# Kernel optimization log

Hardware: AMD Instinct MI355X
Metric: run time of the kernel (lower is better)

## Reference

```python
import jax, jax.numpy as jnp
import numpy as np

B = 8192
I_SIZE = 1024
H_SIZE = 1024
C2 = 2.7183  # module's hard-coded e approximation

def setup_inputs() -> dict:
    key = jax.random.key(0)
    k0, k1, k2, k3, k4 = jax.random.split(key, 5)
    input_tensor = jax.random.uniform(k0, (B, I_SIZE + 1), dtype=jnp.float32)  # last col = dt >= 0
    h_cur = jax.random.normal(k1, (B, H_SIZE), dtype=jnp.float32)
    c_cur = jax.random.normal(k2, (B, H_SIZE), dtype=jnp.float32)
    W_layers = jax.random.normal(k3, (4 * H_SIZE, I_SIZE + H_SIZE), dtype=jnp.float32) * 0.02
    b_layers = jnp.zeros((4 * H_SIZE,), dtype=jnp.float32)
    W_desc = jax.random.normal(k4, (H_SIZE, H_SIZE), dtype=jnp.float32) * 0.02
    b_desc = jnp.zeros((H_SIZE,), dtype=jnp.float32)
    return {"input_tensor": input_tensor, "h_cur": h_cur, "c_cur": c_cur,
            "W_layers": W_layers, "b_layers": b_layers,
            "W_desc": W_desc, "b_desc": b_desc}

def reference(input_tensor, h_cur, c_cur, W_layers, b_layers, W_desc, b_desc):
    x = input_tensor[:, :-1]          # [B, I]
    dt = input_tensor[:, -1:]         # [B, 1]
    # map_elapse_time: T = 1/log(t + e), broadcast over h_size (matmul with ones == broadcast)
    T = 1.0 / jnp.log(dt + C2)        # [B, 1]
    C_ST = jnp.tanh(h_cur @ W_desc.T + b_desc)          # [B, H]
    h_adj = h_cur - C_ST + T * C_ST                     # decayed short-term memory
    combined = jnp.concatenate([x, h_adj], axis=1)      # [B, I+H]
    gates = combined @ W_layers.T + b_layers            # [B, 4H]
    cc_i, cc_f, cc_o, cc_g = jnp.split(gates, 4, axis=1)
    i = jax.nn.sigmoid(cc_i)
    f = jax.nn.sigmoid(cc_f)
    o = jax.nn.sigmoid(cc_o)
    g = jnp.tanh(cc_g)
    c_next = f * c_cur + i * g
    h_next = o * jnp.tanh(c_next)
    return (h_next, c_next)
```

## Files before the change

### kernel.cpp

```cpp
#include <hip/hip_runtime.h>
#include <hip/hip_bf16.h>
#include <math.h>

typedef __bf16 bf16x8 __attribute__((ext_vector_type(8)));
typedef float  f32x4  __attribute__((ext_vector_type(4)));

#define B_ROWS 8192
#define HSZ    1024

#define GLOAD16(gsrc, ldst)                                                          \
  __builtin_amdgcn_global_load_lds((const __attribute__((address_space(1))) void*)(gsrc), \
                                   (__attribute__((address_space(3))) void*)(ldst),  \
                                   16, 0, 0)

__device__ inline unsigned short f2bf(float f) {
  union { float f; unsigned u; } x; x.f = f;
  unsigned r = x.u + 0x7fffu + ((x.u >> 16) & 1u);
  return (unsigned short)(r >> 16);
}

__device__ inline void store4bf(unsigned short* p, float4 v) {
  ushort4 u;
  u.x = f2bf(v.x); u.y = f2bf(v.y); u.z = f2bf(v.z); u.w = f2bf(v.w);
  *(ushort4*)p = u;
}

__device__ inline float sigm(float x) { return 1.0f / (1.0f + __expf(-x)); }

__global__ void k_convert(const float* __restrict__ inp,
                          const float* __restrict__ h,
                          const float* __restrict__ Wl,
                          const float* __restrict__ Wd,
                          unsigned short* __restrict__ comb,
                          unsigned short* __restrict__ Wlb,
                          unsigned short* __restrict__ hb,
                          unsigned short* __restrict__ Wdb,
                          float* __restrict__ Tm1) {
  const long stride = (long)gridDim.x * blockDim.x;
  const long tid0 = (long)blockIdx.x * blockDim.x + threadIdx.x;

  for (long i = tid0; i < (long)B_ROWS * HSZ / 4; i += stride) {
    float4 v = ((const float4*)h)[i];
    store4bf(hb + i * 4, v);
  }
  for (long i = tid0; i < (long)B_ROWS * HSZ / 4; i += stride) {
    long e = i * 4; long b = e >> 10; long c = e & 1023;
    float4 v = *(const float4*)(inp + b * 1025 + c);
    store4bf(comb + b * 2048 + c, v);
  }
  for (long i = tid0; i < 4096L * 2048 / 4; i += stride) {
    float4 v = ((const float4*)Wl)[i];
    store4bf(Wlb + i * 4, v);
  }
  for (long i = tid0; i < 1024L * 1024 / 4; i += stride) {
    float4 v = ((const float4*)Wd)[i];
    store4bf(Wdb + i * 4, v);
  }
  for (long i = tid0; i < B_ROWS; i += stride) {
    float dt = inp[i * 1025 + 1024];
    Tm1[i] = 1.0f / logf(dt + 2.7183f) - 1.0f;
  }
}

__global__ void k_gemm1(const unsigned short* __restrict__ A,
                        const unsigned short* __restrict__ Bm,
                        const float* __restrict__ h,
                        const float* __restrict__ bd,
                        const float* __restrict__ Tm1,
                        unsigned short* __restrict__ comb) {
  const int K = 1024;
  __shared__ __align__(16) unsigned short As[128 * 32];
  __shared__ __align__(16) unsigned short Bs[128 * 32];
  const int tid = threadIdx.x;
  const int lane = tid & 63;
  const int wave = tid >> 6;
  const int wr = wave >> 1, wc = wave & 1;
  const int bRow = blockIdx.x;
  const int bCol = blockIdx.y;

  const int sRow = tid >> 2;
  const int sK = (tid & 3) * 8;
  const unsigned short* aSrc0 = A + (long)(bRow * 128 + sRow) * K + sK;
  const unsigned short* aSrc1 = A + (long)(bRow * 128 + 64 + sRow) * K + sK;
  const unsigned short* bSrc0 = Bm + (long)(bCol * 128 + sRow) * K + sK;
  const unsigned short* bSrc1 = Bm + (long)(bCol * 128 + 64 + sRow) * K + sK;
  unsigned short* aDst0 = As + tid * 8;
  unsigned short* aDst1 = As + 2048 + tid * 8;
  unsigned short* bDst0 = Bs + tid * 8;
  unsigned short* bDst1 = Bs + 2048 + tid * 8;

  f32x4 acc[4][4] = {};
  const int fr = lane & 15, fk = (lane >> 4) * 8;

  for (int k0 = 0; k0 < K; k0 += 32) {
    GLOAD16(aSrc0 + k0, aDst0);
    GLOAD16(aSrc1 + k0, aDst1);
    GLOAD16(bSrc0 + k0, bDst0);
    GLOAD16(bSrc1 + k0, bDst1);
    __syncthreads();
    bf16x8 a[4], b[4];
#pragma unroll
    for (int m = 0; m < 4; m++) a[m] = *(const bf16x8*)(As + (wr * 64 + m * 16 + fr) * 32 + fk);
#pragma unroll
    for (int n = 0; n < 4; n++) b[n] = *(const bf16x8*)(Bs + (wc * 64 + n * 16 + fr) * 32 + fk);
#pragma unroll
    for (int m = 0; m < 4; m++)
#pragma unroll
      for (int n = 0; n < 4; n++)
        acc[m][n] = __builtin_amdgcn_mfma_f32_16x16x32_bf16(a[m], b[n], acc[m][n], 0, 0, 0);
    __syncthreads();
  }

  const int cr = (lane >> 4) * 4;
  const int cc = lane & 15;
#pragma unroll
  for (int m = 0; m < 4; m++)
#pragma unroll
    for (int n = 0; n < 4; n++) {
      const int col = bCol * 128 + wc * 64 + n * 16 + cc;
#pragma unroll
      for (int r = 0; r < 4; r++) {
        const int row = bRow * 128 + wr * 64 + m * 16 + cr + r;
        float v = acc[m][n][r] + bd[col];
        float cst = tanhf(v);
        float hadj = h[(long)row * HSZ + col] + Tm1[row] * cst;
        comb[(long)row * 2048 + 1024 + col] = f2bf(hadj);
      }
    }
}

#define NT2 64
__global__ __launch_bounds__(512, 2)
void k_gemm2_fr(const unsigned short* __restrict__ A,
                const unsigned short* __restrict__ Bm,
                const float* __restrict__ bl,
                const float* __restrict__ c_cur,
                float* __restrict__ out) {
  __shared__ __align__(16) unsigned short lds[4][16384];

  const int tid = threadIdx.x;
  const int lane = tid & 63;
  const int wid = tid >> 6;
  const int wr = wid >> 2;
  const int wc = wid & 3;

  const int bid = blockIdx.x;
  const int xcd = bid & 7;
  const int ii = bid >> 3;
  const int sweep = ii >> 5;
  const int pos = ii & 31;
  const int bRow = xcd * 4 + sweep * 2 + (pos & 1);
  const int bCol = pos >> 1;

  const int sr = tid >> 2;
  const int swsel = (sr >> 1) & 3;
  const int gk = ((tid & 3) ^ swsel) << 3;
  const unsigned short* aBase = A + (long)(bRow * 256 + sr) * 2048 + gk;
  const int rl0 = sr, rl1 = 128 + sr;
  const int grow0 = ((rl0 >> 4) & 3) * 1024 + bCol * 64 + (rl0 >> 6) * 16 + (rl0 & 15);
  const int grow1 = ((rl1 >> 4) & 3) * 1024 + bCol * 64 + (rl1 >> 6) * 16 + (rl1 & 15);
  const unsigned short* bBase0 = Bm + (long)grow0 * 2048 + gk;
  const unsigned short* bBase1 = Bm + (long)grow1 * 2048 + gk;

#define STAGE_A2(slot, tt) { unsigned short* d_ = &lds[slot][0] + tid * 8;        \
    GLOAD16(aBase + (long)(tt) * 32, d_);                                          \
    GLOAD16(aBase + 128L * 2048 + (long)(tt) * 32, d_ + 512 * 8); }
#define STAGE_B2(slot, tt) { unsigned short* d_ = &lds[slot][8192] + tid * 8;     \
    GLOAD16(bBase0 + (long)(tt) * 32, d_);                                         \
    GLOAD16(bBase1 + (long)(tt) * 32, d_ + 512 * 8); }

  const int fr = lane & 15, q = lane >> 4;
  int offA[8], offB[4];
#pragma unroll
  for (int m = 0; m < 8; m++) {
    const int row = wr * 128 + m * 16 + fr;
    offA[m] = row * 32 + ((q ^ ((row >> 1) & 3)) << 3);
  }
#pragma unroll
  for (int n = 0; n < 4; n++) {
    const int row = wc * 64 + n * 16 + fr;
    offB[n] = 8192 + row * 32 + ((q ^ ((row >> 1) & 3)) << 3);
  }

  f32x4 acc[8][4] = {};

  STAGE_A2(0, 0); STAGE_B2(0, 0);
  STAGE_A2(1, 1); STAGE_B2(1, 1);
  STAGE_A2(2, 2); STAGE_B2(2, 2);

#define BODY(t, SLOT, VM, DOSTAGE)                                                   \
  {                                                                                  \
    asm volatile("s_waitcnt vmcnt(" #VM ")" ::: "memory");                           \
    __builtin_amdgcn_s_barrier();                                                    \
    if (DOSTAGE) { STAGE_A2(((t) + 3) & 3, (t) + 3); STAGE_B2(((t) + 3) & 3, (t) + 3); } \
    const unsigned short* buf = &lds[SLOT][0];                                       \
    bf16x8 aF[8], bF[4];                                                             \
    _Pragma("unroll")                                                                \
    for (int n = 0; n < 4; n++) bF[n] = *(const bf16x8*)(buf + offB[n]);             \
    _Pragma("unroll")                                                                \
    for (int m = 0; m < 8; m++) aF[m] = *(const bf16x8*)(buf + offA[m]);             \
    __builtin_amdgcn_s_setprio(1);                                                   \
    _Pragma("unroll")                                                                \
    for (int m = 0; m < 8; m++)                                                      \
      _Pragma("unroll")                                                              \
      for (int n = 0; n < 4; n++)                                                    \
        acc[m][n] = __builtin_amdgcn_mfma_f32_16x16x32_bf16(aF[m], bF[n], acc[m][n], 0, 0, 0); \
    __builtin_amdgcn_s_setprio(0);                                                   \
  }

  for (int t = 0; t < 60; t += 4) {
    BODY(t,     0, 8, true);
    BODY(t + 1, 1, 8, true);
    BODY(t + 2, 2, 8, true);
    BODY(t + 3, 3, 8, true);
  }
  BODY(60, 0, 8, true);
  BODY(61, 1, 8, false);
  BODY(62, 2, 4, false);
  BODY(63, 3, 0, false);
#undef BODY

  const int cr = (lane >> 4) * 4;
  const int cc = lane & 15;
  const int j = bCol * 64 + wc * 16 + cc;
#pragma unroll
  for (int m = 0; m < 8; m++) {
#pragma unroll
    for (int r = 0; r < 4; r++) {
      const int row = bRow * 256 + wr * 128 + m * 16 + cr + r;
      float iv = sigm(acc[m][0][r] + bl[j]);
      float fv = sigm(acc[m][1][r] + bl[1024 + j]);
      float ov = sigm(acc[m][2][r] + bl[2048 + j]);
      float gv = tanhf(acc[m][3][r] + bl[3072 + j]);
      float cn = fv * c_cur[(long)row * HSZ + j] + iv * gv;
      float hn = ov * tanhf(cn);
      out[(long)row * HSZ + j] = hn;
      out[(long)B_ROWS * HSZ + (long)row * HSZ + j] = cn;
    }
  }
}

extern "C" void kernel_launch(void* const* d_in, const int* in_sizes, int n_in,
                              void* d_out, int out_size, void* d_ws, size_t ws_size,
                              hipStream_t stream) {
  const float* inp = (const float*)d_in[0];
  const float* h   = (const float*)d_in[1];
  const float* c   = (const float*)d_in[2];
  const float* Wl  = (const float*)d_in[3];
  const float* bl  = (const float*)d_in[4];
  const float* Wd  = (const float*)d_in[5];
  const float* bd  = (const float*)d_in[6];

  char* ws = (char*)d_ws;
  unsigned short* comb = (unsigned short*)(ws);
  unsigned short* Wlb  = (unsigned short*)(ws + 33554432);
  unsigned short* hb   = (unsigned short*)(ws + 50331648);
  unsigned short* Wdb  = (unsigned short*)(ws + 67108864);
  float*          Tm1  = (float*)(ws + 69206016);
  float*          out  = (float*)d_out;

  hipLaunchKernelGGL(k_convert, dim3(2048), dim3(256), 0, stream,
                     inp, h, Wl, Wd, comb, Wlb, hb, Wdb, Tm1);
  hipLaunchKernelGGL(k_gemm1, dim3(64, 8), dim3(256), 0, stream,
                     hb, Wdb, h, bd, Tm1, comb);
  hipLaunchKernelGGL(k_gemm2_fr, dim3(512), dim3(512), 0, stream,
                     comb, Wlb, bl, c, out);
}
```

Before: 226.2 us.

## Switch gates GEMM to 32x32x16 MFMA with 4x2 wave layout, widen convert loads

Rewrites the main gates GEMM to use 32x32x16 bf16 MFMA instead of 16x16x32, rearranging the waves as 4 rows by 2 columns, each computing 64 rows by 32 columns for every one of the four gates. B-tile staging and the LDS fragment offsets are remapped so each gate's 64 columns sit contiguously. The epilogue is adapted to the 32x32 accumulator layout and hoists the bias loads. The convert kernel also handles 8 elements per thread iteration instead of 4. Larger MFMA tiles need fewer LDS fragment reads per FLOP, at the cost of a new fragment mapping that could hit bank conflicts or be wrong.

```diff
diff --git a/kernel.cpp b/kernel.cpp
--- a/kernel.cpp
+++ b/kernel.cpp
@@ -4,6 +4,7 @@
 
 typedef __bf16 bf16x8 __attribute__((ext_vector_type(8)));
 typedef float  f32x4  __attribute__((ext_vector_type(4)));
+typedef float  f32x16 __attribute__((ext_vector_type(16)));
 
 #define B_ROWS 8192
 #define HSZ    1024
@@ -17,12 +18,6 @@
   union { float f; unsigned u; } x; x.f = f;
   unsigned r = x.u + 0x7fffu + ((x.u >> 16) & 1u);
   return (unsigned short)(r >> 16);
-}
-
-__device__ inline void store4bf(unsigned short* p, float4 v) {
-  ushort4 u;
-  u.x = f2bf(v.x); u.y = f2bf(v.y); u.z = f2bf(v.z); u.w = f2bf(v.w);
-  *(ushort4*)p = u;
 }
 
 __device__ inline float sigm(float x) { return 1.0f / (1.0f + __expf(-x)); }
@@ -39,27 +34,34 @@
   const long stride = (long)gridDim.x * blockDim.x;
   const long tid0 = (long)blockIdx.x * blockDim.x + threadIdx.x;
 
-  for (long i = tid0; i < (long)B_ROWS * HSZ / 4; i += stride) {
-    float4 v = ((const float4*)h)[i];
-    store4bf(hb + i * 4, v);
-  }
-  for (long i = tid0; i < (long)B_ROWS * HSZ / 4; i += stride) {
-    long e = i * 4; long b = e >> 10; long c = e & 1023;
-    float4 v = *(const float4*)(inp + b * 1025 + c);
-    store4bf(comb + b * 2048 + c, v);
-  }
-  for (long i = tid0; i < 4096L * 2048 / 4; i += stride) {
-    float4 v = ((const float4*)Wl)[i];
-    store4bf(Wlb + i * 4, v);
-  }
-  for (long i = tid0; i < 1024L * 1024 / 4; i += stride) {
-    float4 v = ((const float4*)Wd)[i];
-    store4bf(Wdb + i * 4, v);
+#define CNV8(dst, s0, s1) { ushort4 u0, u1;                                   \
+    u0.x = f2bf(s0.x); u0.y = f2bf(s0.y); u0.z = f2bf(s0.z); u0.w = f2bf(s0.w); \
+    u1.x = f2bf(s1.x); u1.y = f2bf(s1.y); u1.z = f2bf(s1.z); u1.w = f2bf(s1.w); \
+    *(ushort4*)(dst) = u0; *(ushort4*)((dst) + 4) = u1; }
+
+  for (long i = tid0; i < (long)B_ROWS * HSZ / 8; i += stride) {
+    float4 v0 = ((const float4*)h)[i * 2], v1 = ((const float4*)h)[i * 2 + 1];
+    CNV8(hb + i * 8, v0, v1);
+  }
+  for (long i = tid0; i < (long)B_ROWS * HSZ / 8; i += stride) {
+    long e = i * 8; long b = e >> 10; long c = e & 1023;
+    const float* s = inp + b * 1025 + c;
+    float4 v0 = *(const float4*)s, v1 = *(const float4*)(s + 4);
+    CNV8(comb + b * 2048 + c, v0, v1);
+  }
+  for (long i = tid0; i < 4096L * 2048 / 8; i += stride) {
+    float4 v0 = ((const float4*)Wl)[i * 2], v1 = ((const float4*)Wl)[i * 2 + 1];
+    CNV8(Wlb + i * 8, v0, v1);
+  }
+  for (long i = tid0; i < 1024L * 1024 / 8; i += stride) {
+    float4 v0 = ((const float4*)Wd)[i * 2], v1 = ((const float4*)Wd)[i * 2 + 1];
+    CNV8(Wdb + i * 8, v0, v1);
   }
   for (long i = tid0; i < B_ROWS; i += stride) {
     float dt = inp[i * 1025 + 1024];
     Tm1[i] = 1.0f / logf(dt + 2.7183f) - 1.0f;
   }
+#undef CNV8
 }
 
 __global__ void k_gemm1(const unsigned short* __restrict__ A,
@@ -131,7 +133,7 @@
 
 #define NT2 64
 __global__ __launch_bounds__(512, 2)
-void k_gemm2_fr(const unsigned short* __restrict__ A,
+void k_gemm2_32(const unsigned short* __restrict__ A,
                 const unsigned short* __restrict__ Bm,
                 const float* __restrict__ bl,
                 const float* __restrict__ c_cur,
@@ -141,8 +143,8 @@
   const int tid = threadIdx.x;
   const int lane = tid & 63;
   const int wid = tid >> 6;
-  const int wr = wid >> 2;
-  const int wc = wid & 3;
+  const int wr = wid >> 1;
+  const int wc = wid & 1;
 
   const int bid = blockIdx.x;
   const int xcd = bid & 7;
@@ -156,33 +158,35 @@
   const int swsel = (sr >> 1) & 3;
   const int gk = ((tid & 3) ^ swsel) << 3;
   const unsigned short* aBase = A + (long)(bRow * 256 + sr) * 2048 + gk;
-  const int rl0 = sr, rl1 = 128 + sr;
-  const int grow0 = ((rl0 >> 4) & 3) * 1024 + bCol * 64 + (rl0 >> 6) * 16 + (rl0 & 15);
-  const int grow1 = ((rl1 >> 4) & 3) * 1024 + bCol * 64 + (rl1 >> 6) * 16 + (rl1 & 15);
+  const int grow0 = (sr >> 6) * 1024 + bCol * 64 + (sr & 63);
+  const int grow1 = (2 + (sr >> 6)) * 1024 + bCol * 64 + (sr & 63);
   const unsigned short* bBase0 = Bm + (long)grow0 * 2048 + gk;
   const unsigned short* bBase1 = Bm + (long)grow1 * 2048 + gk;
 
 #define STAGE_A2(slot, tt) { unsigned short* d_ = &lds[slot][0] + tid * 8;        \
     GLOAD16(aBase + (long)(tt) * 32, d_);                                          \
-    GLOAD16(aBase + 128L * 2048 + (long)(tt) * 32, d_ + 512 * 8); }
+    GLOAD16(aBase + 128L * 2048 + (long)(tt) * 32, d_ + 4096); }
 #define STAGE_B2(slot, tt) { unsigned short* d_ = &lds[slot][8192] + tid * 8;     \
     GLOAD16(bBase0 + (long)(tt) * 32, d_);                                         \
-    GLOAD16(bBase1 + (long)(tt) * 32, d_ + 512 * 8); }
-
-  const int fr = lane & 15, q = lane >> 4;
-  int offA[8], offB[4];
-#pragma unroll
-  for (int m = 0; m < 8; m++) {
-    const int row = wr * 128 + m * 16 + fr;
-    offA[m] = row * 32 + ((q ^ ((row >> 1) & 3)) << 3);
-  }
-#pragma unroll
-  for (int n = 0; n < 4; n++) {
-    const int row = wc * 64 + n * 16 + fr;
-    offB[n] = 8192 + row * 32 + ((q ^ ((row >> 1) & 3)) << 3);
-  }
-
-  f32x4 acc[8][4] = {};
+    GLOAD16(bBase1 + (long)(tt) * 32, d_ + 4096); }
+
+  int offA[2][2], offB[4][2];
+#pragma unroll
+  for (int mt = 0; mt < 2; mt++)
+#pragma unroll
+    for (int ks = 0; ks < 2; ks++) {
+      const int row = wr * 64 + mt * 32 + (lane & 31);
+      offA[mt][ks] = row * 32 + (((2 * ks + (lane >> 5)) ^ ((row >> 1) & 3)) << 3);
+    }
+#pragma unroll
+  for (int g = 0; g < 4; g++)
+#pragma unroll
+    for (int ks = 0; ks < 2; ks++) {
+      const int rl = g * 64 + wc * 32 + (lane & 31);
+      offB[g][ks] = 8192 + rl * 32 + (((2 * ks + (lane >> 5)) ^ ((rl >> 1) & 3)) << 3);
+    }
+
+  f32x16 acc[2][4] = {};
 
   STAGE_A2(0, 0); STAGE_B2(0, 0);
   STAGE_A2(1, 1); STAGE_B2(1, 1);
@@ -194,17 +198,25 @@
     __builtin_amdgcn_s_barrier();                                                    \
     if (DOSTAGE) { STAGE_A2(((t) + 3) & 3, (t) + 3); STAGE_B2(((t) + 3) & 3, (t) + 3); } \
     const unsigned short* buf = &lds[SLOT][0];                                       \
-    bf16x8 aF[8], bF[4];                                                             \
+    bf16x8 aF[2][2], bF[4][2];                                                       \
     _Pragma("unroll")                                                                \
-    for (int n = 0; n < 4; n++) bF[n] = *(const bf16x8*)(buf + offB[n]);             \
+    for (int g = 0; g < 4; g++) {                                                    \
+      bF[g][0] = *(const bf16x8*)(buf + offB[g][0]);                                 \
+      bF[g][1] = *(const bf16x8*)(buf + offB[g][1]);                                 \
+    }                                                                                \
     _Pragma("unroll")                                                                \
-    for (int m = 0; m < 8; m++) aF[m] = *(const bf16x8*)(buf + offA[m]);             \
+    for (int mt = 0; mt < 2; mt++) {                                                 \
+      aF[mt][0] = *(const bf16x8*)(buf + offA[mt][0]);                               \
+      aF[mt][1] = *(const bf16x8*)(buf + offA[mt][1]);                               \
+    }                                                                                \
     __builtin_amdgcn_s_setprio(1);                                                   \
     _Pragma("unroll")                                                                \
-    for (int m = 0; m < 8; m++)                                                      \
+    for (int mt = 0; mt < 2; mt++)                                                   \
       _Pragma("unroll")                                                              \
-      for (int n = 0; n < 4; n++)                                                    \
-        acc[m][n] = __builtin_amdgcn_mfma_f32_16x16x32_bf16(aF[m], bF[n], acc[m][n], 0, 0, 0); \
+      for (int g = 0; g < 4; g++) {                                                  \
+        acc[mt][g] = __builtin_amdgcn_mfma_f32_32x32x16_bf16(aF[mt][0], bF[g][0], acc[mt][g], 0, 0, 0); \
+        acc[mt][g] = __builtin_amdgcn_mfma_f32_32x32x16_bf16(aF[mt][1], bF[g][1], acc[mt][g], 0, 0, 0); \
+      }                                                                              \
     __builtin_amdgcn_s_setprio(0);                                                   \
   }
 
@@ -220,18 +232,18 @@
   BODY(63, 3, 0, false);
 #undef BODY
 
-  const int cr = (lane >> 4) * 4;
-  const int cc = lane & 15;
-  const int j = bCol * 64 + wc * 16 + cc;
-#pragma unroll
-  for (int m = 0; m < 8; m++) {
-#pragma unroll
-    for (int r = 0; r < 4; r++) {
-      const int row = bRow * 256 + wr * 128 + m * 16 + cr + r;
-      float iv = sigm(acc[m][0][r] + bl[j]);
-      float fv = sigm(acc[m][1][r] + bl[1024 + j]);
-      float ov = sigm(acc[m][2][r] + bl[2048 + j]);
-      float gv = tanhf(acc[m][3][r] + bl[3072 + j]);
+  const int j = bCol * 64 + wc * 32 + (lane & 31);
+  const int rb = (lane >> 5) * 4;
+  const float bl0 = bl[j], bl1 = bl[1024 + j], bl2 = bl[2048 + j], bl3 = bl[3072 + j];
+#pragma unroll
+  for (int mt = 0; mt < 2; mt++) {
+#pragma unroll
+    for (int r = 0; r < 16; r++) {
+      const int row = bRow * 256 + wr * 64 + mt * 32 + (r & 3) + 8 * (r >> 2) + rb;
+      float iv = sigm(acc[mt][0][r] + bl0);
+      float fv = sigm(acc[mt][1][r] + bl1);
+      float ov = sigm(acc[mt][2][r] + bl2);
+      float gv = tanhf(acc[mt][3][r] + bl3);
       float cn = fv * c_cur[(long)row * HSZ + j] + iv * gv;
       float hn = ov * tanhf(cn);
       out[(long)row * HSZ + j] = hn;
@@ -263,6 +275,6 @@
                      inp, h, Wl, Wd, comb, Wlb, hb, Wdb, Tm1);
   hipLaunchKernelGGL(k_gemm1, dim3(64, 8), dim3(256), 0, stream,
                      hb, Wdb, h, bd, Tm1, comb);
-  hipLaunchKernelGGL(k_gemm2_fr, dim3(512), dim3(512), 0, stream,
+  hipLaunchKernelGGL(k_gemm2_32, dim3(512), dim3(512), 0, stream,
                      comb, Wlb, bl, c, out);
 }
```

Result: slower. 247.4 us (+9.4%).

## Switch gemm2 to paired-stage pipeline with fewer barriers; widen convert loops

Applied to the files above, without the earlier changes.

The main GEMM moves from a 4-slot ring with prefetch depth 3 and one barrier per K-step to a scheme that processes two K-steps per barrier. It prefetches two stages ahead into the other half of the LDS buffers and drains vmcnt to zero at each pair boundary. The conversion kernel now handles 8 floats per thread iteration instead of 4. The aim is to halve barrier count and cut loop overhead, at the cost of a shallower prefetch and full memory drains that may expose load latency.

```diff
diff --git a/kernel.cpp b/kernel.cpp
--- a/kernel.cpp
+++ b/kernel.cpp
@@ -17,12 +17,6 @@
   union { float f; unsigned u; } x; x.f = f;
   unsigned r = x.u + 0x7fffu + ((x.u >> 16) & 1u);
   return (unsigned short)(r >> 16);
-}
-
-__device__ inline void store4bf(unsigned short* p, float4 v) {
-  ushort4 u;
-  u.x = f2bf(v.x); u.y = f2bf(v.y); u.z = f2bf(v.z); u.w = f2bf(v.w);
-  *(ushort4*)p = u;
 }
 
 __device__ inline float sigm(float x) { return 1.0f / (1.0f + __expf(-x)); }
@@ -39,27 +33,34 @@
   const long stride = (long)gridDim.x * blockDim.x;
   const long tid0 = (long)blockIdx.x * blockDim.x + threadIdx.x;
 
-  for (long i = tid0; i < (long)B_ROWS * HSZ / 4; i += stride) {
-    float4 v = ((const float4*)h)[i];
-    store4bf(hb + i * 4, v);
-  }
-  for (long i = tid0; i < (long)B_ROWS * HSZ / 4; i += stride) {
-    long e = i * 4; long b = e >> 10; long c = e & 1023;
-    float4 v = *(const float4*)(inp + b * 1025 + c);
-    store4bf(comb + b * 2048 + c, v);
-  }
-  for (long i = tid0; i < 4096L * 2048 / 4; i += stride) {
-    float4 v = ((const float4*)Wl)[i];
-    store4bf(Wlb + i * 4, v);
-  }
-  for (long i = tid0; i < 1024L * 1024 / 4; i += stride) {
-    float4 v = ((const float4*)Wd)[i];
-    store4bf(Wdb + i * 4, v);
+#define CNV8(dst, s0, s1) { ushort4 u0, u1;                                   \
+    u0.x = f2bf(s0.x); u0.y = f2bf(s0.y); u0.z = f2bf(s0.z); u0.w = f2bf(s0.w); \
+    u1.x = f2bf(s1.x); u1.y = f2bf(s1.y); u1.z = f2bf(s1.z); u1.w = f2bf(s1.w); \
+    *(ushort4*)(dst) = u0; *(ushort4*)((dst) + 4) = u1; }
+
+  for (long i = tid0; i < (long)B_ROWS * HSZ / 8; i += stride) {
+    float4 v0 = ((const float4*)h)[i * 2], v1 = ((const float4*)h)[i * 2 + 1];
+    CNV8(hb + i * 8, v0, v1);
+  }
+  for (long i = tid0; i < (long)B_ROWS * HSZ / 8; i += stride) {
+    long e = i * 8; long b = e >> 10; long c = e & 1023;
+    const float* s = inp + b * 1025 + c;
+    float4 v0 = *(const float4*)s, v1 = *(const float4*)(s + 4);
+    CNV8(comb + b * 2048 + c, v0, v1);
+  }
+  for (long i = tid0; i < 4096L * 2048 / 8; i += stride) {
+    float4 v0 = ((const float4*)Wl)[i * 2], v1 = ((const float4*)Wl)[i * 2 + 1];
+    CNV8(Wlb + i * 8, v0, v1);
+  }
+  for (long i = tid0; i < 1024L * 1024 / 8; i += stride) {
+    float4 v0 = ((const float4*)Wd)[i * 2], v1 = ((const float4*)Wd)[i * 2 + 1];
+    CNV8(Wdb + i * 8, v0, v1);
   }
   for (long i = tid0; i < B_ROWS; i += stride) {
     float dt = inp[i * 1025 + 1024];
     Tm1[i] = 1.0f / logf(dt + 2.7183f) - 1.0f;
   }
+#undef CNV8
 }
 
 __global__ void k_gemm1(const unsigned short* __restrict__ A,
@@ -131,7 +132,7 @@
 
 #define NT2 64
 __global__ __launch_bounds__(512, 2)
-void k_gemm2_fr(const unsigned short* __restrict__ A,
+void k_gemm2_ww(const unsigned short* __restrict__ A,
                 const unsigned short* __restrict__ Bm,
                 const float* __restrict__ bl,
                 const float* __restrict__ c_cur,
@@ -184,15 +185,9 @@
 
   f32x4 acc[8][4] = {};
 
-  STAGE_A2(0, 0); STAGE_B2(0, 0);
-  STAGE_A2(1, 1); STAGE_B2(1, 1);
-  STAGE_A2(2, 2); STAGE_B2(2, 2);
-
-#define BODY(t, SLOT, VM, DOSTAGE)                                                   \
+#define BODY(t, SLOT)                                                                \
   {                                                                                  \
-    asm volatile("s_waitcnt vmcnt(" #VM ")" ::: "memory");                           \
-    __builtin_amdgcn_s_barrier();                                                    \
-    if (DOSTAGE) { STAGE_A2(((t) + 3) & 3, (t) + 3); STAGE_B2(((t) + 3) & 3, (t) + 3); } \
+    if ((t) + 2 < NT2) { STAGE_A2((SLOT) ^ 2, (t) + 2); STAGE_B2((SLOT) ^ 2, (t) + 2); } \
     const unsigned short* buf = &lds[SLOT][0];                                       \
     bf16x8 aF[8], bF[4];                                                             \
     _Pragma("unroll")                                                                \
@@ -207,18 +202,19 @@
         acc[m][n] = __builtin_amdgcn_mfma_f32_16x16x32_bf16(aF[m], bF[n], acc[m][n], 0, 0, 0); \
     __builtin_amdgcn_s_setprio(0);                                                   \
   }
-
-  for (int t = 0; t < 60; t += 4) {
-    BODY(t,     0, 8, true);
-    BODY(t + 1, 1, 8, true);
-    BODY(t + 2, 2, 8, true);
-    BODY(t + 3, 3, 8, true);
-  }
-  BODY(60, 0, 8, true);
-  BODY(61, 1, 8, false);
-  BODY(62, 2, 4, false);
-  BODY(63, 3, 0, false);
+#define IBOUND() { asm volatile("s_waitcnt vmcnt(0)" ::: "memory"); __builtin_amdgcn_s_barrier(); }
+
+  STAGE_A2(0, 0); STAGE_B2(0, 0);
+  STAGE_A2(1, 1); STAGE_B2(1, 1);
+  IBOUND();
+
+  for (int ip = 0; ip < 16; ++ip) {
+    const int t0 = ip * 4;
+    BODY(t0,     0); BODY(t0 + 1, 1); IBOUND();
+    BODY(t0 + 2, 2); BODY(t0 + 3, 3); IBOUND();
+  }
 #undef BODY
+#undef IBOUND
 
   const int cr = (lane >> 4) * 4;
   const int cc = lane & 15;
@@ -263,6 +259,6 @@
                      inp, h, Wl, Wd, comb, Wlb, hb, Wdb, Tm1);
   hipLaunchKernelGGL(k_gemm1, dim3(64, 8), dim3(256), 0, stream,
                      hb, Wdb, h, bd, Tm1, comb);
-  hipLaunchKernelGGL(k_gemm2_fr, dim3(512), dim3(512), 0, stream,
+  hipLaunchKernelGGL(k_gemm2_ww, dim3(512), dim3(512), 0, stream,
                      comb, Wlb, bl, c, out);
 }
```

New measurement: 228.1 us. About the same (+0.8%).
